# Optimization experiments

Hardware: AMD Instinct MI355X
Metric: run time of the kernel (lower is better)

Reference implementation:

```python
import jax, jax.numpy as jnp
import numpy as np

BETA = 0.5
THR = 1.0
BN_EPS = 1e-5

@jax.custom_vjp
def spike(x):
    # heaviside fire: spk = 1[x > 0]
    return (x > 0).astype(x.dtype)

def _spike_fwd(x):
    return spike(x), x

def _spike_bwd(x, g):
    # snnTorch surrogate.atan(), alpha=2: grad = (alpha/2) / (1 + (pi/2*alpha*x)^2) = 1/(1+(pi*x)^2)
    return (g / (1.0 + (jnp.pi * x) ** 2),)

spike.defvjp(_spike_fwd, _spike_bwd)

def setup_inputs() -> dict:
    key = jax.random.key(0)
    ks = jax.random.split(key, 6)
    B, T, D, O = 512, 128, 512, 10
    data = jax.random.normal(ks[0], (B, T, D), dtype=jnp.float32)
    # deterministic Dropout(0.5) mask in {0, 2} (scaled by 1/keep_prob), time-major
    u = jax.random.uniform(ks[1], (T, B, D), dtype=jnp.float32)
    drop_mask = (u > 0.5).astype(jnp.float32) * 2.0
    W1 = jax.random.normal(ks[2], (D, D), dtype=jnp.float32) / np.sqrt(D)
    b1 = jax.random.normal(ks[3], (D,), dtype=jnp.float32) * 0.01
    gamma = jnp.ones((D,), dtype=jnp.float32)
    bn_beta = jnp.zeros((D,), dtype=jnp.float32)
    W2 = jax.random.normal(ks[4], (O, D), dtype=jnp.float32) / np.sqrt(D)
    b2 = jax.random.normal(ks[5], (O,), dtype=jnp.float32) * 0.01
    return {"data": data, "drop_mask": drop_mask, "W1": W1, "b1": b1,
            "gamma": gamma, "bn_beta": bn_beta, "W2": W2, "b2": b2}

def reference(data, drop_mask, W1, b1, gamma, bn_beta, W2, b2):
    B, T, D = data.shape
    O = W2.shape[0]
    xs = jnp.transpose(data, (1, 0, 2))  # [T, B, D] time-major

    def batchnorm(x):  # training-mode BatchNorm1d over batch dim
        mean = jnp.mean(x, axis=0)
        var = jnp.mean((x - mean) ** 2, axis=0)
        return gamma * (x - mean) * jax.lax.rsqrt(var + BN_EPS) + bn_beta

    def step(carry, inp):
        mem1, spk1, mem2, spk2 = carry
        xt, mt = inp
        cur1 = batchnorm((mt * xt) @ W1.T + b1)          # dropout -> linear -> BN
        mem1 = BETA * mem1 + cur1 - spk1 * THR           # Leaky, subtract reset
        spk1 = spike(mem1 - THR)
        cur2 = spk1 @ W2.T + b2
        mem2 = BETA * mem2 + cur2 - spk2 * THR
        spk2 = spike(mem2 - THR)
        return (mem1, spk1, mem2, spk2), spk2

    init = (jnp.zeros((B, D), data.dtype), jnp.zeros((B, D), data.dtype),
            jnp.zeros((B, O), data.dtype), jnp.zeros((B, O), data.dtype))
    _, spk_rec = jax.lax.scan(step, init, (xs, drop_mask))
    return spk_rec  # [T, B, out_size] == torch.stack(spk_rec)
```

## Files before the change

### kernel.cpp

```cpp
#include <hip/hip_runtime.h>
#include <math.h>

#define B_ 512
#define T_ 128
#define D_ 512
#define O_ 10

typedef unsigned int uint32;
typedef short bf16x8 __attribute__((ext_vector_type(8)));
typedef float f32x4 __attribute__((ext_vector_type(4)));

__device__ __forceinline__ uint32 bf16rne(float f) {
    uint32 u = __float_as_uint(f);
    return (u + 0x7FFFu + ((u >> 16) & 1u)) >> 16;
}
__device__ __forceinline__ float bf16f(uint32 h) { return __uint_as_float(h << 16); }

__global__ __launch_bounds__(256)
void presplitW_kernel(const float* __restrict__ W1, unsigned short* __restrict__ Wsp)
{
    const int idx = blockIdx.x * 256 + threadIdx.x;
    const float4 v = *(const float4*)(W1 + (size_t)idx * 4);
    float vv[4] = {v.x, v.y, v.z, v.w};
    uint32 c0[4], c1[4], c2[4];
#pragma unroll
    for (int i = 0; i < 4; ++i) {
        c0[i] = bf16rne(vv[i]);
        float r = vv[i] - bf16f(c0[i]);
        c1[i] = bf16rne(r);
        float r2 = r - bf16f(c1[i]);
        c2[i] = bf16rne(r2);
    }
    const size_t base = (size_t)idx * 4;
    uint2 w;
    w.x = c0[0] | (c0[1] << 16); w.y = c0[2] | (c0[3] << 16);
    *(uint2*)(Wsp + base) = w;
    w.x = c1[0] | (c1[1] << 16); w.y = c1[2] | (c1[3] << 16);
    *(uint2*)(Wsp + 262144 + base) = w;
    w.x = c2[0] | (c2[1] << 16); w.y = c2[2] | (c2[3] << 16);
    *(uint2*)(Wsp + 524288 + base) = w;
}

#define SPW 34
#define SPL (128*SPW)

__global__ __launch_bounds__(256)
void gemm1_kernel(const float* __restrict__ data, const float* __restrict__ drop,
                  const unsigned short* __restrict__ Wsp, const float* __restrict__ b1,
                  float* __restrict__ hbuf, double* __restrict__ pSum,
                  double* __restrict__ pSq, int t0, int Tc)
{
    __shared__ __align__(16) unsigned short As3[3 * SPL];
    __shared__ __align__(16) unsigned short Ws3[3 * SPL];

    const int tid = threadIdx.x;
    const int bid = blockIdx.x;
    const int xcd = bid & 7;
    const int rest = bid >> 3;
    const int yy = rest & 3;
    const int g = (rest >> 2) * 8 + xcd;

    const int R = g * 128;
    const int tc = R >> 9;
    const int b_base = R & 511;
    const int t = t0 + tc;
    const int d0 = yy * 128;

    const int w = tid >> 6;
    const int lane = tid & 63;
    const int wm = w & 1, wn = w >> 1;
    const int q = lane >> 4, r16 = lane & 15;

    const int lm = tid >> 2;
    const int kg = (tid & 3) * 8;

    f32x4 acc[4][4];
#pragma unroll
    for (int i = 0; i < 4; ++i)
#pragma unroll
        for (int j = 0; j < 4; ++j) acc[i][j] = (f32x4){0.f, 0.f, 0.f, 0.f};

    float4 pd[2][2], pm[2][2];

#define LOADA(K0)                                                                \
    {                                                                            \
        _Pragma("unroll")                                                        \
        for (int i = 0; i < 2; ++i) {                                            \
            const int m = lm + i * 64;                                           \
            const float* dsrc = data + ((size_t)(b_base + m) * T_ + t) * D_ + (K0) + kg; \
            const float* msrc = drop + ((size_t)t * B_ + b_base + m) * D_ + (K0) + kg;   \
            pd[i][0] = *(const float4*)(dsrc);                                   \
            pd[i][1] = *(const float4*)(dsrc + 4);                               \
            pm[i][0] = *(const float4*)(msrc);                                   \
            pm[i][1] = *(const float4*)(msrc + 4);                               \
        }                                                                        \
    }

    LOADA(0)

    for (int k0 = 0; k0 < 512; k0 += 32) {
        uint4 pw[6];
#pragma unroll
        for (int i = 0; i < 6; ++i) {
            const int p = tid + i * 256;
            const int s = p >> 9;
            const int rem = p & 511;
            const int n = rem >> 2;
            const int kg2 = (rem & 3) * 8;
            pw[i] = *(const uint4*)(Wsp + (size_t)s * 262144
                                    + (size_t)(d0 + n) * 512 + k0 + kg2);
        }
#pragma unroll
        for (int i = 0; i < 2; ++i) {
            float vv[8] = {pd[i][0].x*pm[i][0].x, pd[i][0].y*pm[i][0].y,
                           pd[i][0].z*pm[i][0].z, pd[i][0].w*pm[i][0].w,
                           pd[i][1].x*pm[i][1].x, pd[i][1].y*pm[i][1].y,
                           pd[i][1].z*pm[i][1].z, pd[i][1].w*pm[i][1].w};
            uint32 u0[8], u1[8], u2[8];
#pragma unroll
            for (int e = 0; e < 8; ++e) {
                u0[e] = bf16rne(vv[e]);
                const float r = vv[e] - bf16f(u0[e]);
                u1[e] = bf16rne(r);
                const float r2 = r - bf16f(u1[e]);
                u2[e] = bf16rne(r2);
            }
            const int dst = (lm + i * 64) * SPW + kg;
            uint4 pk;
            pk.x = u0[0]|(u0[1]<<16); pk.y = u0[2]|(u0[3]<<16);
            pk.z = u0[4]|(u0[5]<<16); pk.w = u0[6]|(u0[7]<<16);
            *(uint4*)(&As3[dst]) = pk;
            pk.x = u1[0]|(u1[1]<<16); pk.y = u1[2]|(u1[3]<<16);
            pk.z = u1[4]|(u1[5]<<16); pk.w = u1[6]|(u1[7]<<16);
            *(uint4*)(&As3[SPL + dst]) = pk;
            pk.x = u2[0]|(u2[1]<<16); pk.y = u2[2]|(u2[3]<<16);
            pk.z = u2[4]|(u2[5]<<16); pk.w = u2[6]|(u2[7]<<16);
            *(uint4*)(&As3[2*SPL + dst]) = pk;
        }
#pragma unroll
        for (int i = 0; i < 6; ++i) {
            const int p = tid + i * 256;
            const int s = p >> 9;
            const int rem = p & 511;
            const int n = rem >> 2;
            const int kg2 = (rem & 3) * 8;
            *(uint4*)(&Ws3[s * SPL + n * SPW + kg2]) = pw[i];
        }
        __syncthreads();

        bf16x8 af[4][3], bfr[4][3];
#pragma unroll
        for (int mt = 0; mt < 4; ++mt)
#pragma unroll
            for (int s = 0; s < 3; ++s)
                af[mt][s] = *(const bf16x8*)(&As3[s*SPL + (wm*64 + mt*16 + r16)*SPW + q*8]);
#pragma unroll
        for (int nt = 0; nt < 4; ++nt)
#pragma unroll
            for (int s = 0; s < 3; ++s)
                bfr[nt][s] = *(const bf16x8*)(&Ws3[s*SPL + (wn*64 + nt*16 + r16)*SPW + q*8]);

        if (k0 + 32 < 512) LOADA(k0 + 32)

#define PRODUCT(SA, SB)                                                          \
        {                                                                        \
            _Pragma("unroll")                                                    \
            for (int mt = 0; mt < 4; ++mt) {                                     \
                _Pragma("unroll")                                                \
                for (int nt = 0; nt < 4; ++nt)                                   \
                    acc[mt][nt] = __builtin_amdgcn_mfma_f32_16x16x32_bf16(       \
                        af[mt][SA], bfr[nt][SB], acc[mt][nt], 0, 0, 0);          \
            }                                                                    \
        }
        PRODUCT(0, 0)
        PRODUCT(0, 1)
        PRODUCT(1, 0)
        PRODUCT(1, 1)
        PRODUCT(0, 2)
        PRODUCT(2, 0)
#undef PRODUCT
        __syncthreads();
    }

    float b1c[4];
#pragma unroll
    for (int nt = 0; nt < 4; ++nt) b1c[nt] = b1[d0 + wn*64 + nt*16 + r16];

    double sd[4], sq[4];
#pragma unroll
    for (int nt = 0; nt < 4; ++nt) { sd[nt] = 0.0; sq[nt] = 0.0; }

#pragma unroll
    for (int mt = 0; mt < 4; ++mt)
#pragma unroll
        for (int r = 0; r < 4; ++r) {
            const int row = R + wm*64 + mt*16 + q*4 + r;
            float* op = hbuf + (size_t)row * D_ + d0 + wn*64 + r16;
#pragma unroll
            for (int nt = 0; nt < 4; ++nt) {
                const float hf = acc[mt][nt][r] + b1c[nt];
                op[nt*16] = hf;
                const double dh = (double)hf;
                sd[nt] += dh;
                sq[nt] = fma(dh, dh, sq[nt]);
            }
        }
#pragma unroll
    for (int nt = 0; nt < 4; ++nt) {
        sd[nt] += __shfl_xor(sd[nt], 16); sd[nt] += __shfl_xor(sd[nt], 32);
        sq[nt] += __shfl_xor(sq[nt], 16); sq[nt] += __shfl_xor(sq[nt], 32);
    }
    double* dsh = (double*)&As3[0];
    __syncthreads();
    if (q == 0) {
#pragma unroll
        for (int nt = 0; nt < 4; ++nt) {
            dsh[(w*64 + nt*16 + r16)*2 + 0] = sd[nt];
            dsh[(w*64 + nt*16 + r16)*2 + 1] = sq[nt];
        }
    }
    __syncthreads();
    if (tid < 128) {
        const int col = tid;
        const int gg = col >> 6, c = col & 63;
        const double S = dsh[((2*gg)*64 + c)*2 + 0] + dsh[((2*gg+1)*64 + c)*2 + 0];
        const double Q = dsh[((2*gg)*64 + c)*2 + 1] + dsh[((2*gg+1)*64 + c)*2 + 1];
        const int bt = b_base >> 7;
        pSum[((size_t)(bt*Tc + tc))*D_ + d0 + col] = S;
        pSq [((size_t)(bt*Tc + tc))*D_ + d0 + col] = Q;
    }
}

__global__ __launch_bounds__(256)
void finalize_kernel(const double* __restrict__ pSum, const double* __restrict__ pSq,
                     const float* __restrict__ gamma, const float* __restrict__ bn_beta,
                     float* __restrict__ scaleArr, float* __restrict__ shiftArr, int Tc)
{
    const int tc = blockIdx.x;
    const int d = blockIdx.y * 256 + threadIdx.x;
    double S = 0.0, Q = 0.0;
#pragma unroll
    for (int bt = 0; bt < 4; ++bt) {
        S += pSum[((size_t)(bt * Tc + tc)) * D_ + d];
        Q += pSq [((size_t)(bt * Tc + tc)) * D_ + d];
    }
    const double mean = S / (double)B_;
    const double var  = Q / (double)B_ - mean * mean;
    const double rs   = 1.0 / sqrt(var + 1e-5);
    const double gm   = (double)gamma[d] * rs;
    scaleArr[tc * D_ + d] = (float)gm;
    shiftArr[tc * D_ + d] = (float)((double)bn_beta[d] - gm * mean);
}

__global__ __launch_bounds__(256)
void scanA_kernel(const float* __restrict__ hbuf, const float* __restrict__ scaleArr,
                  const float* __restrict__ shiftArr, unsigned short* __restrict__ spk,
                  float* __restrict__ sMem1, float* __restrict__ sSpk1, int t0, int Tc)
{
    const int e = blockIdx.x * 256 + threadIdx.x;
    const int b = e >> 9;
    const int d = e & 511;

    float m1, s1;
    if (t0 == 0) { m1 = 0.f; s1 = 0.f; }
    else { m1 = sMem1[e]; s1 = sSpk1[e]; }

    float hv = hbuf[e];
    float sc = scaleArr[d];
    float sf = shiftArr[d];

    for (int tc = 0; tc < Tc; ++tc) {
        float hvN, scN, sfN;
        if (tc + 1 < Tc) {
            hvN = hbuf[(size_t)(tc + 1) * (B_ * D_) + e];
            scN = scaleArr[(tc + 1) * D_ + d];
            sfN = shiftArr[(tc + 1) * D_ + d];
        }
        const float cur1 = fmaf(sc, hv, sf);
        m1 = fmaf(0.5f, m1, cur1) - s1;
        s1 = ((m1 - 1.0f) > 0.f) ? 1.f : 0.f;
        spk[(size_t)tc * (B_ * D_) + e] = (s1 == 1.f) ? (unsigned short)0x3F80u
                                                      : (unsigned short)0u;
        hv = hvN; sc = scN; sf = sfN;
    }

    sMem1[e] = m1;
    sSpk1[e] = s1;
}

__global__ __launch_bounds__(256)
void gemm2_kernel(const unsigned short* __restrict__ spk, const float* __restrict__ W2,
                  const float* __restrict__ b2, float* __restrict__ cur2)
{
    const int tid = threadIdx.x;
    const int w = tid >> 6, lane = tid & 63;
    const int rowBase = blockIdx.x * 16 + w * 4;

    float w2r[O_][8];
#pragma unroll
    for (int o = 0; o < O_; ++o) {
        const float4 wa = *(const float4*)(W2 + o * D_ + lane * 8);
        const float4 wb = *(const float4*)(W2 + o * D_ + lane * 8 + 4);
        w2r[o][0] = wa.x; w2r[o][1] = wa.y; w2r[o][2] = wa.z; w2r[o][3] = wa.w;
        w2r[o][4] = wb.x; w2r[o][5] = wb.y; w2r[o][6] = wb.z; w2r[o][7] = wb.w;
    }
    float b2v[O_];
#pragma unroll
    for (int o = 0; o < O_; ++o) b2v[o] = b2[o];

    for (int rr = 0; rr < 4; ++rr) {
        const int row = rowBase + rr;
        const uint4 sv = *(const uint4*)(spk + (size_t)row * D_ + lane * 8);
        float f[8];
        f[0] = bf16f(sv.x & 0xFFFFu); f[1] = bf16f(sv.x >> 16);
        f[2] = bf16f(sv.y & 0xFFFFu); f[3] = bf16f(sv.y >> 16);
        f[4] = bf16f(sv.z & 0xFFFFu); f[5] = bf16f(sv.z >> 16);
        f[6] = bf16f(sv.w & 0xFFFFu); f[7] = bf16f(sv.w >> 16);
        float p[O_];
#pragma unroll
        for (int o = 0; o < O_; ++o) {
            float v = f[0] * w2r[o][0];
#pragma unroll
            for (int j = 1; j < 8; ++j) v = fmaf(f[j], w2r[o][j], v);
            p[o] = v;
        }
#pragma unroll
        for (int o = 0; o < O_; ++o) {
#pragma unroll
            for (int off = 32; off > 0; off >>= 1)
                p[o] += __shfl_xor(p[o], off);
        }
        float outv = 0.f;
#pragma unroll
        for (int o = 0; o < O_; ++o)
            if (lane == o) outv = p[o] + b2v[o];
        if (lane < O_)
            cur2[(size_t)row * O_ + lane] = outv;
    }
}

__global__ __launch_bounds__(256)
void scanB_kernel(const float* __restrict__ cur2, float* __restrict__ out,
                  float* __restrict__ sMem2, float* __restrict__ sSpk2, int t0, int Tc)
{
    const int idx = blockIdx.x * 256 + threadIdx.x;
    float mem2, spk2;
    if (t0 == 0) { mem2 = 0.f; spk2 = 0.f; }
    else { mem2 = sMem2[idx]; spk2 = sSpk2[idx]; }

    float v[4], vn[4];
#pragma unroll
    for (int j = 0; j < 4; ++j) v[j] = cur2[(size_t)j * (B_ * O_) + idx];

    for (int tg = 0; tg < Tc; tg += 4) {
        if (tg + 4 < Tc) {
#pragma unroll
            for (int j = 0; j < 4; ++j)
                vn[j] = cur2[(size_t)(tg + 4 + j) * (B_ * O_) + idx];
        }
#pragma unroll
        for (int j = 0; j < 4; ++j) {
            mem2 = fmaf(0.5f, mem2, v[j]) - spk2;
            spk2 = ((mem2 - 1.0f) > 0.f) ? 1.f : 0.f;
            out[(size_t)(t0 + tg + j) * (B_ * O_) + idx] = spk2;
        }
#pragma unroll
        for (int j = 0; j < 4; ++j) v[j] = vn[j];
    }
    sMem2[idx] = mem2;
    sSpk2[idx] = spk2;
}

extern "C" void kernel_launch(void* const* d_in, const int* in_sizes, int n_in,
                              void* d_out, int out_size, void* d_ws, size_t ws_size,
                              hipStream_t stream) {
    const float* data    = (const float*)d_in[0];
    const float* drop    = (const float*)d_in[1];
    const float* W1      = (const float*)d_in[2];
    const float* b1      = (const float*)d_in[3];
    const float* gamma   = (const float*)d_in[4];
    const float* bn_beta = (const float*)d_in[5];
    const float* W2      = (const float*)d_in[6];
    const float* b2      = (const float*)d_in[7];
    float* out = (float*)d_out;

    const size_t fixedBytes = 1572864 + 2*1048576 + 2*20480;
    const size_t perT = 1048576 + 524288 + 20480 + 4096 + 32768;
    int Tc = T_;
    while (Tc > 2 && fixedBytes + (size_t)Tc * perT > ws_size) Tc >>= 1;

    char* p = (char*)d_ws;
    double* pSum    = (double*)p; p += (size_t)4 * Tc * D_ * 8;
    double* pSq     = (double*)p; p += (size_t)4 * Tc * D_ * 8;
    float* hbuf     = (float*)p; p += (size_t)Tc * B_ * D_ * 4;
    float* scaleArr = (float*)p; p += (size_t)Tc * D_ * 4;
    float* shiftArr = (float*)p; p += (size_t)Tc * D_ * 4;
    float* sMem1    = (float*)p; p += (size_t)B_ * D_ * 4;
    float* sSpk1    = (float*)p; p += (size_t)B_ * D_ * 4;
    float* sMem2    = (float*)p; p += (size_t)B_ * O_ * 4;
    float* sSpk2    = (float*)p; p += (size_t)B_ * O_ * 4;
    float* cur2     = (float*)p; p += (size_t)Tc * B_ * O_ * 4;
    unsigned short* Wsp = (unsigned short*)p; p += (size_t)3 * D_ * D_ * 2;
    unsigned short* spk = (unsigned short*)p; p += (size_t)Tc * B_ * D_ * 2;

    presplitW_kernel<<<256, 256, 0, stream>>>(W1, Wsp);

    for (int t0 = 0; t0 < T_; t0 += Tc) {
        gemm1_kernel<<<Tc * 16, 256, 0, stream>>>(data, drop, Wsp, b1, hbuf,
                                                  pSum, pSq, t0, Tc);
        finalize_kernel<<<dim3(Tc, D_ / 256), 256, 0, stream>>>(
            pSum, pSq, gamma, bn_beta, scaleArr, shiftArr, Tc);
        scanA_kernel<<<(B_ * D_) / 256, 256, 0, stream>>>(hbuf, scaleArr, shiftArr, spk,
                                                          sMem1, sSpk1, t0, Tc);
        gemm2_kernel<<<Tc * 32, 256, 0, stream>>>(spk, W2, b2, cur2);
        scanB_kernel<<<20, 256, 0, stream>>>(cur2, out, sMem2, sSpk2, t0, Tc);
    }
}
```

Measured before the change: 622.2 us.

## Bit-pack spike tensor via ballot and drop register prefetch in gemm1

scanA now writes spikes as 64-bit ballot masks instead of bf16 values, and gemm2 unpacks the bits. This cuts spike traffic between the two kernels by a factor of 16. gemm1 drops its register double-buffered prefetch of the activation tiles, loads the W tiles inline, and changes the LDS row pitch from 34 to 40. That lowers register pressure but exposes global load latency before each barrier. The workspace size estimate is reduced to match the smaller spike buffer.

```diff
diff --git a/kernel.cpp b/kernel.cpp
--- a/kernel.cpp
+++ b/kernel.cpp
@@ -7,6 +7,7 @@
 #define O_ 10
 
 typedef unsigned int uint32;
+typedef unsigned long long uint64;
 typedef short bf16x8 __attribute__((ext_vector_type(8)));
 typedef float f32x4 __attribute__((ext_vector_type(4)));
 
@@ -41,7 +42,7 @@
     *(uint2*)(Wsp + 524288 + base) = w;
 }
 
-#define SPW 34
+#define SPW 40
 #define SPL (128*SPW)
 
 __global__ __launch_bounds__(256)
@@ -71,51 +72,26 @@
     const int wm = w & 1, wn = w >> 1;
     const int q = lane >> 4, r16 = lane & 15;
 
-    const int lm = tid >> 2;
-    const int kg = (tid & 3) * 8;
-
     f32x4 acc[4][4];
 #pragma unroll
     for (int i = 0; i < 4; ++i)
 #pragma unroll
         for (int j = 0; j < 4; ++j) acc[i][j] = (f32x4){0.f, 0.f, 0.f, 0.f};
 
-    float4 pd[2][2], pm[2][2];
-
-#define LOADA(K0)                                                                \
-    {                                                                            \
-        _Pragma("unroll")                                                        \
-        for (int i = 0; i < 2; ++i) {                                            \
-            const int m = lm + i * 64;                                           \
-            const float* dsrc = data + ((size_t)(b_base + m) * T_ + t) * D_ + (K0) + kg; \
-            const float* msrc = drop + ((size_t)t * B_ + b_base + m) * D_ + (K0) + kg;   \
-            pd[i][0] = *(const float4*)(dsrc);                                   \
-            pd[i][1] = *(const float4*)(dsrc + 4);                               \
-            pm[i][0] = *(const float4*)(msrc);                                   \
-            pm[i][1] = *(const float4*)(msrc + 4);                               \
-        }                                                                        \
-    }
-
-    LOADA(0)
-
     for (int k0 = 0; k0 < 512; k0 += 32) {
-        uint4 pw[6];
-#pragma unroll
-        for (int i = 0; i < 6; ++i) {
+#pragma unroll
+        for (int i = 0; i < 2; ++i) {
             const int p = tid + i * 256;
-            const int s = p >> 9;
-            const int rem = p & 511;
-            const int n = rem >> 2;
-            const int kg2 = (rem & 3) * 8;
-            pw[i] = *(const uint4*)(Wsp + (size_t)s * 262144
-                                    + (size_t)(d0 + n) * 512 + k0 + kg2);
-        }
-#pragma unroll
-        for (int i = 0; i < 2; ++i) {
-            float vv[8] = {pd[i][0].x*pm[i][0].x, pd[i][0].y*pm[i][0].y,
-                           pd[i][0].z*pm[i][0].z, pd[i][0].w*pm[i][0].w,
-                           pd[i][1].x*pm[i][1].x, pd[i][1].y*pm[i][1].y,
-                           pd[i][1].z*pm[i][1].z, pd[i][1].w*pm[i][1].w};
+            const int m = p >> 2;
+            const int kg = (p & 3) * 8;
+            const float* dsrc = data + ((size_t)(b_base + m) * T_ + t) * D_ + k0 + kg;
+            const float* msrc = drop + ((size_t)t * B_ + b_base + m) * D_ + k0 + kg;
+            const float4 dv0 = *(const float4*)(dsrc);
+            const float4 dv1 = *(const float4*)(dsrc + 4);
+            const float4 mv0 = *(const float4*)(msrc);
+            const float4 mv1 = *(const float4*)(msrc + 4);
+            float vv[8] = {dv0.x*mv0.x, dv0.y*mv0.y, dv0.z*mv0.z, dv0.w*mv0.w,
+                           dv1.x*mv1.x, dv1.y*mv1.y, dv1.z*mv1.z, dv1.w*mv1.w};
             uint32 u0[8], u1[8], u2[8];
 #pragma unroll
             for (int e = 0; e < 8; ++e) {
@@ -125,7 +101,7 @@
                 const float r2 = r - bf16f(u1[e]);
                 u2[e] = bf16rne(r2);
             }
-            const int dst = (lm + i * 64) * SPW + kg;
+            const int dst = m * SPW + kg;
             uint4 pk;
             pk.x = u0[0]|(u0[1]<<16); pk.y = u0[2]|(u0[3]<<16);
             pk.z = u0[4]|(u0[5]<<16); pk.w = u0[6]|(u0[7]<<16);
@@ -143,8 +119,10 @@
             const int s = p >> 9;
             const int rem = p & 511;
             const int n = rem >> 2;
-            const int kg2 = (rem & 3) * 8;
-            *(uint4*)(&Ws3[s * SPL + n * SPW + kg2]) = pw[i];
+            const int kg = (rem & 3) * 8;
+            const uint4 pk = *(const uint4*)(Wsp + (size_t)s * 262144
+                                             + (size_t)(d0 + n) * 512 + k0 + kg);
+            *(uint4*)(&Ws3[s * SPL + n * SPW + kg]) = pk;
         }
         __syncthreads();
 
@@ -159,8 +137,6 @@
 #pragma unroll
             for (int s = 0; s < 3; ++s)
                 bfr[nt][s] = *(const bf16x8*)(&Ws3[s*SPL + (wn*64 + nt*16 + r16)*SPW + q*8]);
-
-        if (k0 + 32 < 512) LOADA(k0 + 32)
 
 #define PRODUCT(SA, SB)                                                          \
         {                                                                        \
@@ -254,12 +230,14 @@
 
 __global__ __launch_bounds__(256)
 void scanA_kernel(const float* __restrict__ hbuf, const float* __restrict__ scaleArr,
-                  const float* __restrict__ shiftArr, unsigned short* __restrict__ spk,
+                  const float* __restrict__ shiftArr, uint64* __restrict__ spkM,
                   float* __restrict__ sMem1, float* __restrict__ sSpk1, int t0, int Tc)
 {
     const int e = blockIdx.x * 256 + threadIdx.x;
     const int b = e >> 9;
     const int d = e & 511;
+    const int lane = threadIdx.x & 63;
+    const int mword = (e >> 6);
 
     float m1, s1;
     if (t0 == 0) { m1 = 0.f; s1 = 0.f; }
@@ -279,8 +257,11 @@
         const float cur1 = fmaf(sc, hv, sf);
         m1 = fmaf(0.5f, m1, cur1) - s1;
         s1 = ((m1 - 1.0f) > 0.f) ? 1.f : 0.f;
-        spk[(size_t)tc * (B_ * D_) + e] = (s1 == 1.f) ? (unsigned short)0x3F80u
-                                                      : (unsigned short)0u;
+
+        const uint64 mask = __ballot(s1 == 1.f);
+        if (lane == 0)
+            spkM[(size_t)tc * (B_ * 8) + mword] = mask;
+
         hv = hvN; sc = scN; sf = sfN;
     }
 
@@ -289,7 +270,7 @@
 }
 
 __global__ __launch_bounds__(256)
-void gemm2_kernel(const unsigned short* __restrict__ spk, const float* __restrict__ W2,
+void gemm2_kernel(const uint64* __restrict__ spkM, const float* __restrict__ W2,
                   const float* __restrict__ b2, float* __restrict__ cur2)
 {
     const int tid = threadIdx.x;
@@ -310,12 +291,12 @@
 
     for (int rr = 0; rr < 4; ++rr) {
         const int row = rowBase + rr;
-        const uint4 sv = *(const uint4*)(spk + (size_t)row * D_ + lane * 8);
+        const uint64 mk = spkM[(size_t)row * 8 + (lane >> 3)];
+        const uint32 byte = (uint32)(mk >> ((lane & 7) * 8)) & 0xFFu;
         float f[8];
-        f[0] = bf16f(sv.x & 0xFFFFu); f[1] = bf16f(sv.x >> 16);
-        f[2] = bf16f(sv.y & 0xFFFFu); f[3] = bf16f(sv.y >> 16);
-        f[4] = bf16f(sv.z & 0xFFFFu); f[5] = bf16f(sv.z >> 16);
-        f[6] = bf16f(sv.w & 0xFFFFu); f[7] = bf16f(sv.w >> 16);
+#pragma unroll
+        for (int j = 0; j < 8; ++j)
+            f[j] = (byte & (1u << j)) ? 1.0f : 0.0f;
         float p[O_];
 #pragma unroll
         for (int o = 0; o < O_; ++o) {
@@ -385,7 +366,7 @@
     float* out = (float*)d_out;
 
     const size_t fixedBytes = 1572864 + 2*1048576 + 2*20480;
-    const size_t perT = 1048576 + 524288 + 20480 + 4096 + 32768;
+    const size_t perT = 1048576 + 32768 + 20480 + 4096 + 32768;
     int Tc = T_;
     while (Tc > 2 && fixedBytes + (size_t)Tc * perT > ws_size) Tc >>= 1;
 
@@ -401,7 +382,7 @@
     float* sSpk2    = (float*)p; p += (size_t)B_ * O_ * 4;
     float* cur2     = (float*)p; p += (size_t)Tc * B_ * O_ * 4;
     unsigned short* Wsp = (unsigned short*)p; p += (size_t)3 * D_ * D_ * 2;
-    unsigned short* spk = (unsigned short*)p; p += (size_t)Tc * B_ * D_ * 2;
+    uint64* spkM    = (uint64*)p; p += (size_t)Tc * B_ * 8 * 8;
 
     presplitW_kernel<<<256, 256, 0, stream>>>(W1, Wsp);
 
@@ -410,9 +391,9 @@
                                                   pSum, pSq, t0, Tc);
         finalize_kernel<<<dim3(Tc, D_ / 256), 256, 0, stream>>>(
             pSum, pSq, gamma, bn_beta, scaleArr, shiftArr, Tc);
-        scanA_kernel<<<(B_ * D_) / 256, 256, 0, stream>>>(hbuf, scaleArr, shiftArr, spk,
+        scanA_kernel<<<(B_ * D_) / 256, 256, 0, stream>>>(hbuf, scaleArr, shiftArr, spkM,
                                                           sMem1, sSpk1, t0, Tc);
-        gemm2_kernel<<<Tc * 32, 256, 0, stream>>>(spk, W2, b2, cur2);
+        gemm2_kernel<<<Tc * 32, 256, 0, stream>>>(spkM, W2, b2, cur2);
         scanB_kernel<<<20, 256, 0, stream>>>(cur2, out, sMem2, sSpk2, t0, Tc);
     }
 }
```

New measurement: 541.0 us. 13.0% less time.
